# Kernel tuning notes

Hardware: AMD Instinct MI355X
Metric: run time of the kernel (lower is better)

The kernel has to match this reference:

```python
import jax, jax.numpy as jnp
import numpy as np

HIDDEN = 256
HEAD = 256
GAMMA = 0.96875
SCALE_BASE = 512  # default scale_base in the standard XPOS module


def xpos_apply(x, offset=0, downscale=False):
    """xpos rotary embedding. x: (B, S, H) with H even."""
    B, S, H = x.shape
    half = H // 2
    dt = x.dtype
    pos = jnp.arange(offset, offset + S, dtype=dt)  # (S,)
    # per-channel xpos scale: ((2i + 0.4H) / (1.4H)) ** (pos / scale_base)
    base_scale = (jnp.arange(0, H, 2, dtype=dt) + 0.4 * H) / (1.4 * H)  # (half,)
    scale = base_scale[None, :] ** (pos[:, None] / SCALE_BASE)          # (S, half)
    if downscale:
        scale = 1.0 / scale
    inv_freq = 1.0 / (10000.0 ** (jnp.arange(half, dtype=dt) / half))   # (half,)
    sinusoid = pos[:, None] * inv_freq[None, :]                         # (S, half)
    sin = jnp.sin(sinusoid) * scale
    cos = jnp.cos(sinusoid) * scale
    # duplicate-interleave columns to width H
    sin2 = jnp.repeat(sin, 2, axis=-1)  # (S, H)
    cos2 = jnp.repeat(cos, 2, axis=-1)
    # rotate_every_two
    x1 = x[..., 0::2]
    x2 = x[..., 1::2]
    rot = jnp.stack([-x2, x1], axis=-1).reshape(x.shape)
    return x * cos2[None] + rot * sin2[None]


def decay_mask(S, dtype):
    n = jnp.arange(S)
    diff = n[:, None] - n[None, :]
    # gamma^(i-j) for i>=j else 0 (clamp exponent to avoid huge values under the mask)
    D = jnp.where(diff >= 0,
                  jnp.asarray(GAMMA, dtype) ** jnp.maximum(diff, 0).astype(dtype),
                  jnp.zeros((), dtype))
    return D


def setup_inputs() -> dict:
    key = jax.random.key(0)
    k1, k2, k3, k4 = jax.random.split(key, 4)
    B, N, S = 2, 8, 2048
    X = jax.random.normal(k1, (B, N, S, HIDDEN), dtype=jnp.float32)
    # kaiming-uniform-ish init: uniform in [-1/sqrt(fan_in), 1/sqrt(fan_in)]
    bound = 1.0 / np.sqrt(HIDDEN)
    W_Q = jax.random.uniform(k2, (HIDDEN, HEAD), jnp.float32, -bound, bound)
    W_K = jax.random.uniform(k3, (HIDDEN, HEAD), jnp.float32, -bound, bound)
    W_V = jax.random.uniform(k4, (HIDDEN, HEAD), jnp.float32, -bound, bound)
    return {"X": X, "W_Q": W_Q, "W_K": W_K, "W_V": W_V}


def reference(X, W_Q, W_K, W_V):
    B, N, S, H = X.shape
    Q = X @ W_Q  # (B, N, S, head)
    K = X @ W_K
    V = X @ W_V
    hd = Q.shape[-1]
    Q = xpos_apply(Q.reshape(B * N, S, hd)).reshape(B, N, S, hd)
    K = xpos_apply(K.reshape(B * N, S, hd), downscale=True).reshape(B, N, S, hd)
    D = decay_mask(S, X.dtype)  # (S, S)
    scores = jnp.einsum('bnsh,bnth->bnst', Q, K) * D  # (B, N, S, S)
    return scores @ V  # (B, N, S, v_dim)
```

## Files before the change

### kernel.cpp

```cpp
#include <hip/hip_runtime.h>
#include <hip/hip_bf16.h>


#define S_LEN 2048
#define HD 256
#define BN 16

typedef _Float16 half8 __attribute__((ext_vector_type(8)));
typedef _Float16 half4 __attribute__((ext_vector_type(4)));
typedef _Float16 half2v __attribute__((ext_vector_type(2)));
typedef float floatx16 __attribute__((ext_vector_type(16)));

__device__ __forceinline__ void gl_lds16(const void* g, void* l) {
  __builtin_amdgcn_global_load_lds(
      (const __attribute__((address_space(1))) unsigned int*)(unsigned long long)g,
      (__attribute__((address_space(3))) unsigned int*)(unsigned int)(unsigned long long)l,
      16, 0, 0);
}

__global__ __launch_bounds__(256) void prep_kernel(
    const float* __restrict__ WQ, const float* __restrict__ WK,
    const float* __restrict__ WV, _Float16* __restrict__ WT,
    _Float16* __restrict__ TBL) {
  const int b = blockIdx.x;
  const int tid = threadIdx.x;
  if (b < 1024) {
    const int idx = b * 256 + tid;
    const int i2 = idx & 127;
    const int pos = idx >> 7;
    float inv_freq = exp2f(-(float)i2 * (13.287712379549449f / 128.0f));
    float lbase = log2f(((float)(2 * i2) + 102.4f) / 358.4f);
    float ang = (float)pos * inv_freq;
    float sn, cs;
    sincosf(ang, &sn, &cs);
    float scl = exp2f((float)pos * (1.0f / 512.0f) * lbase);
    float rscl = 1.0f / scl;
    half2v tq, tk;
    tq[0] = (_Float16)(cs * scl);  tq[1] = (_Float16)(sn * scl);
    tk[0] = (_Float16)(cs * rscl); tk[1] = (_Float16)(sn * rscl);
    *(half2v*)&TBL[(long)idx * 2] = tq;
    *(half2v*)&TBL[(long)(262144 + idx) * 2] = tk;
    return;
  }
  __shared__ _Float16 trans[64][72];
  const int bb = b - 1024;
  const int w = bb >> 4;
  const int tk = ((bb & 15) & 3) * 64;
  const int tn = ((bb & 15) >> 2) * 64;
  const float* W = (w == 0) ? WQ : (w == 1) ? WK : WV;
#pragma unroll
  for (int u = 0; u < 4; ++u) {
    int idx = u * 256 + tid;
    int k = idx >> 4;
    int nq = (idx & 15) * 4;
    float4 v = *(const float4*)&W[(tk + k) * HD + tn + nq];
    trans[nq + 0][k] = (_Float16)v.x;
    trans[nq + 1][k] = (_Float16)v.y;
    trans[nq + 2][k] = (_Float16)v.z;
    trans[nq + 3][k] = (_Float16)v.w;
  }
  __syncthreads();
#pragma unroll
  for (int u = 0; u < 2; ++u) {
    int idx = u * 256 + tid;
    int n = idx >> 3;
    int kq = (idx & 7) * 8;
    *(uint4*)&WT[((long)w * HD + tn + n) * HD + tk + kq] = *(const uint4*)&trans[n][kq];
  }
}

__global__ __launch_bounds__(512) void gemm_qkv_kernel(
    const float* __restrict__ X, const _Float16* __restrict__ WT,
    const _Float16* __restrict__ TBL,
    _Float16* __restrict__ Q, _Float16* __restrict__ K,
    _Float16* __restrict__ VT) {
  __shared__ __align__(16) unsigned char smem[66560];
  unsigned char* ep = smem + 32768;

  const int tid = threadIdx.x;
  const int lane = tid & 63;
  const int w = tid >> 6;
  const int l31 = lane & 31;
  const int lh = lane >> 5;
  const int m0 = blockIdx.x * 64;

#pragma unroll
  for (int i = 0; i < 4; ++i) {
    int id = i * 512 + tid;
    int row = id >> 5, c = id & 31;
    int p = c ^ (row & 31);
    const float4* s = (const float4*)&X[(long)(m0 + row) * HD + c * 8];
    float4 v0 = s[0], v1 = s[1];
    half8 h;
    h[0] = (_Float16)v0.x; h[1] = (_Float16)v0.y;
    h[2] = (_Float16)v0.z; h[3] = (_Float16)v0.w;
    h[4] = (_Float16)v1.x; h[5] = (_Float16)v1.y;
    h[6] = (_Float16)v1.z; h[7] = (_Float16)v1.w;
    *(half8*)(smem + row * 512 + p * 16) = h;
  }
  __syncthreads();

  const int bn = m0 >> 11;
  const int srow0 = m0 & (S_LEN - 1);
  const int ncol0 = w * 32;

  for (int wsel = 0; wsel < 3; ++wsel) {
    const _Float16* Wb = WT + (long)wsel * HD * HD;
    floatx16 acc[2];
#pragma unroll
    for (int mt = 0; mt < 2; ++mt)
#pragma unroll
      for (int e = 0; e < 16; ++e) acc[mt][e] = 0.f;

    half8 b[5];
#pragma unroll
    for (int pk = 0; pk < 5; ++pk)
      b[pk] = *(const half8*)(Wb + (long)(ncol0 + l31) * HD + pk * 16 + lh * 8);
#pragma unroll
    for (int ks16 = 0; ks16 < 16; ++ks16) {
      const int slot = ks16 % 5;
      int p = (ks16 * 2 + lh) ^ l31;
      half8 af0 = *(const half8*)(smem + l31 * 512 + p * 16);
      half8 af1 = *(const half8*)(smem + (32 + l31) * 512 + p * 16);
      acc[0] = __builtin_amdgcn_mfma_f32_32x32x16_f16(af0, b[slot], acc[0], 0, 0, 0);
      acc[1] = __builtin_amdgcn_mfma_f32_32x32x16_f16(af1, b[slot], acc[1], 0, 0, 0);
      if (ks16 + 5 < 16)
        b[slot] = *(const half8*)(Wb + (long)(ncol0 + l31) * HD +
                                  (ks16 + 5) * 16 + lh * 8);
    }

    if (wsel < 2) {
      const int col = ncol0 + l31;
#pragma unroll
      for (int mt = 0; mt < 2; ++mt)
#pragma unroll
        for (int reg = 0; reg < 16; ++reg) {
          int rmap = (reg & 3) + 8 * (reg >> 2) + 4 * lh;
          *(_Float16*)(ep + (mt * 32 + rmap) * 528 + col * 2) =
              (_Float16)acc[mt][reg];
        }
      __syncthreads();
      _Float16* o = wsel ? K : Q;
      const _Float16* tb_base = TBL + (long)wsel * 2048 * 128 * 2;
#pragma unroll
      for (int u = 0; u < 4; ++u) {
        int id = u * 512 + tid;
        int row = id >> 5;
        int cq = (id & 31) * 8;
        half8 x = *(const half8*)(ep + row * 528 + cq * 2);
        half8 t = *(const half8*)&tb_base[((long)(srow0 + row) * 128 + (cq >> 1)) * 2];
        half8 y;
        y[0] = x[0] * t[0] - x[1] * t[1];
        y[1] = x[1] * t[0] + x[0] * t[1];
        y[2] = x[2] * t[2] - x[3] * t[3];
        y[3] = x[3] * t[2] + x[2] * t[3];
        y[4] = x[4] * t[4] - x[5] * t[5];
        y[5] = x[5] * t[4] + x[4] * t[5];
        y[6] = x[6] * t[6] - x[7] * t[7];
        y[7] = x[7] * t[6] + x[6] * t[7];
        *(half8*)&o[(long)(m0 + row) * HD + cq] = y;
      }
      __syncthreads();
    } else {
      __syncthreads();
      _Float16 (*vt)[72] = (_Float16(*)[72])smem;
      const int h = ncol0 + l31;
#pragma unroll
      for (int mt = 0; mt < 2; ++mt)
#pragma unroll
        for (int reg = 0; reg < 16; ++reg) {
          int rmap = (reg & 3) + 8 * (reg >> 2) + 4 * lh;
          vt[h][mt * 32 + rmap] = (_Float16)acc[mt][reg];
        }
      __syncthreads();
#pragma unroll
      for (int u = 0; u < 4; ++u) {
        int id = u * 512 + tid;
        int hh = id >> 3, sj = (id & 7) * 8;
        *(uint4*)&VT[((long)bn * HD + hh) * S_LEN + srow0 + sj] = *(const uint4*)&vt[hh][sj];
      }
    }
  }
}

__global__ __launch_bounds__(256) void retention_kernel(
    const _Float16* __restrict__ Q, const _Float16* __restrict__ K,
    const _Float16* __restrict__ VT, float* __restrict__ out) {
  __shared__ __align__(16) unsigned char smem[74752];
  unsigned char* ksb = smem;
  unsigned char* vsb = smem + 32768;
  _Float16 (*sc)[72] = (_Float16(*)[72])(smem + 65536);

  const int tid = threadIdx.x;
  const int lane = tid & 63;
  const int w = tid >> 6;
  const int l31 = lane & 31;
  const int lh = lane >> 5;
  const int qtile = w >> 1;
  const int ttile = w & 1;
  const int hhalf = w & 1;

  const int L = blockIdx.x;
  const int head = L & 15;
  const int g4 = L >> 4;
  const int qt = (g4 < 16) ? (31 - g4) : (g4 - 16);
  const int q0 = qt * 64;

  const _Float16* Qh = Q + (long)head * S_LEN * HD;
  const _Float16* Kh = K + (long)head * S_LEN * HD;
  const _Float16* VTh = VT + (long)head * HD * S_LEN;

  half8 qf[16];
  {
    const _Float16* qrow = Qh + (long)(q0 + qtile * 32 + l31) * HD + lh * 8;
#pragma unroll
    for (int ks16 = 0; ks16 < 16; ++ks16)
      qf[ks16] = *(const half8*)(qrow + ks16 * 16);
  }

  floatx16 acc[4];
#pragma unroll
  for (int nt = 0; nt < 4; ++nt)
#pragma unroll
    for (int e = 0; e < 16; ++e) acc[nt][e] = 0.f;

  const float LG = -0.0458036896f;
  float Cg[16];
#pragma unroll
  for (int g = 0; g < 4; ++g)
#pragma unroll
    for (int r = 0; r < 4; ++r) Cg[4 * g + r] = exp2f(-(float)(8 * g + r) * LG);

#define STAGE_K(T0)                                                        \
  {                                                                        \
    _Pragma("unroll") for (int j = 0; j < 8; ++j) {                        \
      int li = w * 8 + j;                                                  \
      int row = li * 2 + lh;                                               \
      int c = l31 ^ (row & 31);                                            \
      gl_lds16(Kh + (long)((T0) + row) * HD + c * 8, ksb + li * 1024);     \
    }                                                                      \
  }
#define STAGE_V(T0)                                                        \
  {                                                                        \
    _Pragma("unroll") for (int j = 0; j < 8; ++j) {                        \
      int li = w * 8 + j;                                                  \
      int row = li * 8 + (lane >> 3);                                      \
      int c = (lane & 7) ^ (row & 7);                                      \
      gl_lds16(VTh + (long)row * S_LEN + (T0) + c * 8, vsb + li * 1024);   \
    }                                                                      \
  }

  STAGE_K(0);
  STAGE_V(0);

  for (int kt = 0; kt <= qt; ++kt) {
    const int t0 = kt * 64;
    asm volatile("s_waitcnt vmcnt(0)" ::: "memory");
    __syncthreads();

    floatx16 s;
#pragma unroll
    for (int e = 0; e < 16; ++e) s[e] = 0.f;
    {
      const unsigned char* kbase = ksb + (ttile * 32 + l31) * 512;
#pragma unroll
      for (int ks16 = 0; ks16 < 16; ++ks16) {
        int p = (ks16 * 2 + lh) ^ l31;
        half8 a = *(const half8*)(kbase + p * 16);
        s = __builtin_amdgcn_mfma_f32_32x32x16_f16(a, qf[ks16], s, 0, 0, 0);
      }
    }

    {
      const int qg = q0 + qtile * 32 + l31;
      const int tb = t0 + ttile * 32 + 4 * lh;
      const int dd = qg - tb;
      const float E = exp2f((float)dd * LG);
#pragma unroll
      for (int g = 0; g < 4; ++g) {
        half4 h4;
#pragma unroll
        for (int r = 0; r < 4; ++r) {
          int o = 8 * g + r;
          float wv = (dd >= o) ? E * Cg[4 * g + r] : 0.f;
          h4[r] = (_Float16)(s[4 * g + r] * wv);
        }
        *(half4*)&sc[qtile * 32 + l31][ttile * 32 + 4 * lh + 8 * g] = h4;
      }
    }
    __syncthreads();

    if (kt < qt) STAGE_K(t0 + 64);

#pragma unroll
    for (int kst = 0; kst < 4; ++kst) {
      half8 a = *(const half8*)&sc[qtile * 32 + l31][kst * 16 + lh * 8];
#pragma unroll
      for (int nt = 0; nt < 4; ++nt) {
        int h = hhalf * 128 + nt * 32 + l31;
        int p = (kst * 2 + lh) ^ (h & 7);
        half8 b = *(const half8*)(vsb + h * 128 + p * 16);
        acc[nt] = __builtin_amdgcn_mfma_f32_32x32x16_f16(a, b, acc[nt], 0, 0, 0);
      }
    }
    asm volatile("s_waitcnt vmcnt(0)" ::: "memory");
    __syncthreads();

    if (kt < qt) STAGE_V(t0 + 64);
  }

  const long rbase = (long)head * S_LEN + q0 + qtile * 32;
#pragma unroll
  for (int nt = 0; nt < 4; ++nt) {
    int col = hhalf * 128 + nt * 32 + l31;
#pragma unroll
    for (int reg = 0; reg < 16; ++reg) {
      int rmap = (reg & 3) + 8 * (reg >> 2) + 4 * lh;
      out[(rbase + rmap) * HD + col] = acc[nt][reg];
    }
  }
}

extern "C" void kernel_launch(void* const* d_in, const int* in_sizes, int n_in,
                              void* d_out, int out_size, void* d_ws, size_t ws_size,
                              hipStream_t stream) {
  const float* X  = (const float*)d_in[0];
  const float* WQ = (const float*)d_in[1];
  const float* WK = (const float*)d_in[2];
  const float* WV = (const float*)d_in[3];
  float* out = (float*)d_out;

  _Float16* Qh = (_Float16*)d_ws;
  _Float16* Kh = Qh + (size_t)BN * S_LEN * HD;
  _Float16* VTh = Kh + (size_t)BN * S_LEN * HD;
  _Float16* WT = VTh + (size_t)BN * S_LEN * HD;
  _Float16* TBL = WT + (size_t)3 * HD * HD;

  prep_kernel<<<dim3(1072), dim3(256), 0, stream>>>(WQ, WK, WV, WT, TBL);
  gemm_qkv_kernel<<<dim3((BN * S_LEN) / 64), dim3(512), 0, stream>>>(
      X, WT, TBL, Qh, Kh, VTh);
  retention_kernel<<<dim3(512), dim3(256), 0, stream>>>(Qh, Kh, VTh, out);
}
```

Measured before the change: 173.4 us.

## Fuse Q projection and xpos into retention kernel, drop Q round-trip

Moves the Q projection out of the QKV GEMM kernel and into the retention kernel. Each retention block now loads its 64 rows of X, runs the Q GEMM with MFMA, applies the xpos rotation and keeps Q fragments in registers. This removes the write and re-read of the fp16 Q tensor and one third of the GEMM kernel's work. The cost is a per-block GEMM prologue in the retention kernel, extra register pressure from the accumulators, and extra LDS syncs before the main loop.

After: 198.8 us. 1.15x slower.

```diff
diff --git a/kernel.cpp b/kernel.cpp
--- a/kernel.cpp
+++ b/kernel.cpp
@@ -69,11 +69,10 @@
   }
 }
 
-__global__ __launch_bounds__(512) void gemm_qkv_kernel(
+__global__ __launch_bounds__(512) void gemm_kv_kernel(
     const float* __restrict__ X, const _Float16* __restrict__ WT,
     const _Float16* __restrict__ TBL,
-    _Float16* __restrict__ Q, _Float16* __restrict__ K,
-    _Float16* __restrict__ VT) {
+    _Float16* __restrict__ K, _Float16* __restrict__ VT) {
   __shared__ __align__(16) unsigned char smem[66560];
   unsigned char* ep = smem + 32768;
 
@@ -104,7 +103,7 @@
   const int srow0 = m0 & (S_LEN - 1);
   const int ncol0 = w * 32;
 
-  for (int wsel = 0; wsel < 3; ++wsel) {
+  for (int wsel = 1; wsel < 3; ++wsel) {
     const _Float16* Wb = WT + (long)wsel * HD * HD;
     floatx16 acc[2];
 #pragma unroll
@@ -140,8 +139,7 @@
               (_Float16)acc[mt][reg];
         }
       __syncthreads();
-      _Float16* o = wsel ? K : Q;
-      const _Float16* tb_base = TBL + (long)wsel * 2048 * 128 * 2;
+      const _Float16* tb_base = TBL + (long)1 * 2048 * 128 * 2;
 #pragma unroll
       for (int u = 0; u < 4; ++u) {
         int id = u * 512 + tid;
@@ -158,7 +156,7 @@
         y[5] = x[5] * t[4] + x[4] * t[5];
         y[6] = x[6] * t[6] - x[7] * t[7];
         y[7] = x[7] * t[6] + x[6] * t[7];
-        *(half8*)&o[(long)(m0 + row) * HD + cq] = y;
+        *(half8*)&K[(long)(m0 + row) * HD + cq] = y;
       }
       __syncthreads();
     } else {
@@ -184,12 +182,15 @@
 }
 
 __global__ __launch_bounds__(256) void retention_kernel(
-    const _Float16* __restrict__ Q, const _Float16* __restrict__ K,
-    const _Float16* __restrict__ VT, float* __restrict__ out) {
+    const float* __restrict__ X, const _Float16* __restrict__ WT,
+    const _Float16* __restrict__ TBL,
+    const _Float16* __restrict__ K, const _Float16* __restrict__ VT,
+    float* __restrict__ out) {
   __shared__ __align__(16) unsigned char smem[74752];
   unsigned char* ksb = smem;
   unsigned char* vsb = smem + 32768;
   _Float16 (*sc)[72] = (_Float16(*)[72])(smem + 65536);
+  unsigned char* ep = smem + 32768;
 
   const int tid = threadIdx.x;
   const int lane = tid & 63;
@@ -206,16 +207,94 @@
   const int qt = (g4 < 16) ? (31 - g4) : (g4 - 16);
   const int q0 = qt * 64;
 
-  const _Float16* Qh = Q + (long)head * S_LEN * HD;
   const _Float16* Kh = K + (long)head * S_LEN * HD;
   const _Float16* VTh = VT + (long)head * HD * S_LEN;
 
   half8 qf[16];
   {
-    const _Float16* qrow = Qh + (long)(q0 + qtile * 32 + l31) * HD + lh * 8;
-#pragma unroll
-    for (int ks16 = 0; ks16 < 16; ++ks16)
-      qf[ks16] = *(const half8*)(qrow + ks16 * 16);
+#pragma unroll
+    for (int i = 0; i < 8; ++i) {
+      int id = i * 256 + tid;
+      int row = id >> 5, c = id & 31;
+      int p = c ^ (row & 31);
+      const float4* s =
+          (const float4*)&X[((long)head * S_LEN + q0 + row) * HD + c * 8];
+      float4 v0 = s[0], v1 = s[1];
+      half8 h;
+      h[0] = (_Float16)v0.x; h[1] = (_Float16)v0.y;
+      h[2] = (_Float16)v0.z; h[3] = (_Float16)v0.w;
+      h[4] = (_Float16)v1.x; h[5] = (_Float16)v1.y;
+      h[6] = (_Float16)v1.z; h[7] = (_Float16)v1.w;
+      *(half8*)(ksb + row * 512 + p * 16) = h;
+    }
+    __syncthreads();
+
+    const int ncol0 = w * 64;
+    const _Float16* Wb = WT;
+    floatx16 qa[2][2];
+#pragma unroll
+    for (int mt = 0; mt < 2; ++mt)
+#pragma unroll
+      for (int nt = 0; nt < 2; ++nt)
+#pragma unroll
+        for (int e = 0; e < 16; ++e) qa[mt][nt][e] = 0.f;
+    half8 b[5][2];
+#pragma unroll
+    for (int pk = 0; pk < 5; ++pk)
+#pragma unroll
+      for (int nt = 0; nt < 2; ++nt)
+        b[pk][nt] = *(const half8*)(Wb + (long)(ncol0 + nt * 32 + l31) * HD +
+                                    pk * 16 + lh * 8);
+#pragma unroll
+    for (int ks16 = 0; ks16 < 16; ++ks16) {
+      const int slot = ks16 % 5;
+      int p = (ks16 * 2 + lh) ^ l31;
+      half8 af0 = *(const half8*)(ksb + l31 * 512 + p * 16);
+      half8 af1 = *(const half8*)(ksb + (32 + l31) * 512 + p * 16);
+#pragma unroll
+      for (int nt = 0; nt < 2; ++nt) {
+        qa[0][nt] = __builtin_amdgcn_mfma_f32_32x32x16_f16(af0, b[slot][nt], qa[0][nt], 0, 0, 0);
+        qa[1][nt] = __builtin_amdgcn_mfma_f32_32x32x16_f16(af1, b[slot][nt], qa[1][nt], 0, 0, 0);
+      }
+      if (ks16 + 5 < 16) {
+#pragma unroll
+        for (int nt = 0; nt < 2; ++nt)
+          b[slot][nt] = *(const half8*)(Wb + (long)(ncol0 + nt * 32 + l31) * HD +
+                                        (ks16 + 5) * 16 + lh * 8);
+      }
+    }
+#pragma unroll
+    for (int mt = 0; mt < 2; ++mt)
+#pragma unroll
+      for (int nt = 0; nt < 2; ++nt) {
+        int col = ncol0 + nt * 32 + l31;
+#pragma unroll
+        for (int reg = 0; reg < 16; ++reg) {
+          int rmap = (reg & 3) + 8 * (reg >> 2) + 4 * lh;
+          *(_Float16*)(ep + (mt * 32 + rmap) * 528 + col * 2) =
+              (_Float16)qa[mt][nt][reg];
+        }
+      }
+    __syncthreads();
+
+    const int qrow = qtile * 32 + l31;
+    const long pos = (long)(q0 + qrow);
+#pragma unroll
+    for (int ks16 = 0; ks16 < 16; ++ks16) {
+      half8 x = *(const half8*)(ep + qrow * 528 + (ks16 * 16 + lh * 8) * 2);
+      half8 t = *(const half8*)&TBL[(pos * 128 + ks16 * 8 + lh * 4) * 2];
+      half8 y;
+      y[0] = x[0] * t[0] - x[1] * t[1];
+      y[1] = x[1] * t[0] + x[0] * t[1];
+      y[2] = x[2] * t[2] - x[3] * t[3];
+      y[3] = x[3] * t[2] + x[2] * t[3];
+      y[4] = x[4] * t[4] - x[5] * t[5];
+      y[5] = x[5] * t[4] + x[4] * t[5];
+      y[6] = x[6] * t[6] - x[7] * t[7];
+      y[7] = x[7] * t[6] + x[6] * t[7];
+      qf[ks16] = y;
+    }
+    __syncthreads();
   }
 
   floatx16 acc[4];
@@ -337,7 +416,8 @@
   _Float16* TBL = WT + (size_t)3 * HD * HD;
 
   prep_kernel<<<dim3(1072), dim3(256), 0, stream>>>(WQ, WK, WV, WT, TBL);
-  gemm_qkv_kernel<<<dim3((BN * S_LEN) / 64), dim3(512), 0, stream>>>(
-      X, WT, TBL, Qh, Kh, VTh);
-  retention_kernel<<<dim3(512), dim3(256), 0, stream>>>(Qh, Kh, VTh, out);
+  gemm_kv_kernel<<<dim3((BN * S_LEN) / 64), dim3(512), 0, stream>>>(
+      X, WT, TBL, Kh, VTh);
+  retention_kernel<<<dim3(512), dim3(256), 0, stream>>>(
+      X, WT, TBL, Kh, VTh, out);
 }
```
